# Performance work log

Hardware: AMD Instinct MI355X
Metric: run time of the kernel (lower is better)

Reference implementation:

```python
import jax, jax.numpy as jnp
import numpy as np

K = 3
PAD = 1
GROUPS = 1
BASES = 16


def _conv2d(x, w, b, pad):
    # x: (B, Cin, H, W), w: (Cout, Cin, kh, kw) NCHW/OIHW
    out = jax.lax.conv_general_dilated(
        x, w, window_strides=(1, 1), padding=[(pad, pad), (pad, pad)],
        dimension_numbers=("NCHW", "OIHW", "NCHW"))
    return out + b[None, :, None, None]


def setup_inputs() -> dict:
    key = jax.random.key(0)
    ks = jax.random.split(key, 5)
    B, C, H, Wd = 4, 64, 128, 128
    x = jax.random.normal(ks[0], (B, C, H, Wd), dtype=jnp.float32)
    # basis weight: (1, groups, out_c/g * in_c/g * k^2, bases)
    J = (C // GROUPS) * K * K
    Og = C // GROUPS
    W = jax.random.normal(ks[1], (1, GROUPS, Og * J, BASES), dtype=jnp.float32) * 0.05
    pw = jax.random.normal(ks[2], (BASES, C, 1, 1), dtype=jnp.float32) * 0.05
    pb = jnp.zeros((BASES,), dtype=jnp.float32)
    cw = jax.random.normal(ks[3], (BASES, BASES, 3, 3), dtype=jnp.float32) * 0.05
    cb = jnp.zeros((BASES,), dtype=jnp.float32)
    return {"x": x, "W": W, "pw": pw, "pb": pb, "cw": cw, "cb": cb}


def reference(x, W, pw, pb, cw, cb):
    B, C, H, Wd = x.shape
    P = H * Wd
    g = GROUPS
    Og = C // g          # out channels per group (out_c == in_c here)
    J = (C // g) * K * K  # unfolded patch length per group

    # predictor: 1x1 conv -> relu -> 3x3 conv  => para: (B, bases, P)
    para = _conv2d(x, pw, pb, 0)
    para = jax.nn.relu(para)
    para = _conv2d(para, cw, cb, 1)
    para = para.reshape(B, BASES, P)

    # unfold (im2col): feature dim ordered (c, kh, kw) like F.unfold
    xu = jax.lax.conv_general_dilated_patches(
        x, filter_shape=(K, K), window_strides=(1, 1),
        padding=[(PAD, PAD), (PAD, PAD)])  # (B, C*K*K, H, W)
    xu = xu.reshape(B, g, J, P)

    # per-pixel dynamic weights: weight[b,g,o,j,p] = sum_e Wb[g,o,j,e] * para[b,e,p]
    # out[b,g,o,p] = sum_j weight * xu  -- reassociate: contract j first (small E)
    Wb = W.reshape(g, Og, J, BASES)
    t = jnp.einsum('goje,bgjp->bgoep', Wb, xu)      # (B, g, Og, E, P)
    out = jnp.einsum('bgoep,bep->bgop', t, para)    # (B, g, Og, P)
    return out.reshape(B, C, H, Wd)
```

## Files before the change

kernel.cpp:

```cpp
#include <hip/hip_runtime.h>

typedef __attribute__((ext_vector_type(8))) short short8;
typedef __attribute__((ext_vector_type(8))) __bf16 bf16x8;
typedef __attribute__((ext_vector_type(4))) float f32x4;

#define B_ 4
#define C_ 64
#define H_ 128
#define W_ 128
#define P_ (H_*W_)
#define E_ 16

#define OFF_XT   0u
#define XT_BYTES (4u*130u*130u*64u*2u)
#define OFF_A    8652800u
#define OFF_R1   9832448u

__device__ inline unsigned short f2bf(float f) {
    union { float f; unsigned u; } v; v.f = f;
    unsigned r = v.u + 0x7FFF + ((v.u >> 16) & 1);
    return (unsigned short)(r >> 16);
}

__global__ __launch_bounds__(256) void k_prep(const float* __restrict__ x,
                                              unsigned short* __restrict__ xt,
                                              const float* __restrict__ pw,
                                              const float* __restrict__ pb,
                                              float* __restrict__ r1,
                                              const float* __restrict__ Wsrc,
                                              unsigned short* __restrict__ A) {
    __shared__ float smem[9216];
    int t = threadIdx.x;
    if (blockIdx.x < 256) {
        float* lpw = smem;
        float* lpb = smem + 1024;
        for (int lin = t; lin < 1024; lin += 256) lpw[lin] = pw[lin];
        if (t < 16) lpb[t] = pb[t];
        __syncthreads();

        int rowid = blockIdx.x * 2 + (t >> 7);
        int b = rowid >> 7, y = rowid & 127;
        int tt = t & 127;

        const float* src = x + (size_t)b * C_ * P_ + y * W_ + tt;
        unsigned short* dst = xt + ((size_t)(b * 130 + y + 1) * 130 + tt + 1) * 64;
        float s[16];
#pragma unroll
        for (int e = 0; e < 16; ++e) s[e] = lpb[e];
#pragma unroll
        for (int i = 0; i < 8; ++i) {
            short8 v;
#pragma unroll
            for (int j = 0; j < 8; ++j) {
                float xv = src[(size_t)(i * 8 + j) * P_];
                v[j] = (short)f2bf(xv);
#pragma unroll
                for (int e = 0; e < 16; ++e) s[e] = fmaf(lpw[e * 64 + i * 8 + j], xv, s[e]);
            }
            ((short8*)dst)[i] = v;
        }
        float* rd = r1 + (size_t)b * 16 * P_ + y * 128 + tt;
#pragma unroll
        for (int e = 0; e < 16; ++e) rd[(size_t)e * P_] = fmaxf(s[e], 0.f);

        short8 z = {0,0,0,0,0,0,0,0};
        if (tt < 16) {
            int col = (tt >> 3) * 129, i = tt & 7;
            unsigned short* bp = xt + ((size_t)(b * 130 + y + 1) * 130 + col) * 64;
            ((short8*)bp)[i] = z;
        }
        if (y == 0 || y == 127) {
            int prow = (y == 0) ? 0 : 129;
            unsigned short* rp = xt + (size_t)(b * 130 + prow) * 130 * 64;
            for (int ci = tt; ci < 1040; ci += 128) ((short8*)rp)[ci] = z;
        }
    } else {
        int o = blockIdx.x - 256;
        const float* src = Wsrc + (size_t)o * 9216;
        for (int lin = t; lin < 9216; lin += 256) smem[lin] = src[lin];
        __syncthreads();
        int g = o >> 2, f = o & 3;
        unsigned short* dst = A + ((size_t)g * 72 + f) * 512;
        for (int lin = t; lin < 9216; lin += 256) {
            int ks = lin >> 9, rem = lin & 511;
            int lane = rem >> 3, j = rem & 7;
            int llo = lane & 15, lhi = lane >> 4;
            int col = ks * 32 + lhi * 8 + j;
            int tap = col >> 6, c = col & 63;
            dst[(size_t)ks * 2048 + rem] = f2bf(smem[(c * 9 + tap) * 16 + llo]);
        }
    }
}

__global__ __launch_bounds__(256, 2) void k_main(const unsigned short* __restrict__ xt,
                                                 const unsigned short* __restrict__ A,
                                                 const float* __restrict__ r1,
                                                 const float* __restrict__ cw,
                                                 const float* __restrict__ cb,
                                                 float* __restrict__ out) {
    __shared__ unsigned short lds[3 * 130 * 64];
    __shared__ float lcw2[2304];
    __shared__ float parald[16 * 128];
    int r = blockIdx.x;
    int xcd = r & 7;
    int yl = r >> 3;
    int rowid = xcd * 64 + yl;
    int b = rowid >> 7, y = rowid & 127;

    int tid = threadIdx.x;
    int wave = tid >> 6, lane = tid & 63, lhi = lane >> 4, llo = lane & 15;

    const unsigned short* xrow = xt + (size_t)(b * 130 + y) * 130 * 64;
    for (int ci = tid; ci < 3120; ci += 256) {
        int row = ci / 1040, rem = ci - row * 1040;
        int xx = rem >> 3, cc = rem & 7;
        short8 v = *(const short8*)(xrow + ((size_t)row * 130 + xx) * 64 + cc * 8);
        int lb = row * 16640 + xx * 128 + ((cc * 16) ^ ((xx & 7) << 4));
        *(short8*)((char*)lds + lb) = v;
    }
    for (int lin = tid; lin < 2304; lin += 256) {
        int ep = lin / 144, rem = lin - ep * 144;
        int tap = rem >> 4, e = rem & 15;
        lcw2[lin] = cw[(e * 16 + ep) * 9 + tap];
    }
    __syncthreads();

    {
        int px = tid & 127, eg = tid >> 7;
        const float* r1b = r1 + (size_t)b * 16 * P_;
        float s[8];
#pragma unroll
        for (int ee = 0; ee < 8; ++ee) s[ee] = cb[eg * 8 + ee];
        for (int dy = 0; dy < 3; ++dy) {
            int yy = y + dy - 1;
            if (yy < 0 || yy > 127) continue;
            for (int dx = 0; dx < 3; ++dx) {
                int xx = px + dx - 1;
                if (xx < 0 || xx > 127) continue;
                int tap = dy * 3 + dx;
                const float* rq = r1b + yy * 128 + xx;
                const float* cwt = lcw2 + tap * 16 + eg * 8;
#pragma unroll
                for (int ep = 0; ep < 16; ++ep) {
                    float v = rq[(size_t)ep * P_];
                    const float* cc = cwt + ep * 144;
#pragma unroll
                    for (int ee = 0; ee < 8; ++ee) s[ee] = fmaf(cc[ee], v, s[ee]);
                }
            }
        }
#pragma unroll
        for (int ee = 0; ee < 8; ++ee) parald[(eg * 8 + ee) * 128 + px] = s[ee];
    }
    __syncthreads();

    float* po = out + (size_t)b * 64 * P_ + y * 128;

    int qv[2][3];
#pragma unroll
    for (int kw = 0; kw < 3; ++kw) {
        int rowi = llo + kw;
        int base0 = rowi * 128 + ((lhi * 16) ^ ((rowi & 7) << 4));
        qv[0][kw] = base0;
        qv[1][kw] = base0 ^ 64;
    }
    const char* ldsc = (const char*)lds;

#define PF_AF(dst, KS) do { \
    _Pragma("unroll") \
    for (int f_ = 0; f_ < 4; ++f_) \
        dst[f_] = *(const bf16x8*)(Agl + (KS) * 2048 + f_ * 512); \
    __builtin_amdgcn_sched_barrier(0); \
} while (0)

#define HALF(AFU, AFP, PFKS, PAR, KW) do { \
    PF_AF(AFP, PFKS); \
    const char* bp = bprow + qv[PAR][KW]; \
    bf16x8 bf[8]; \
    _Pragma("unroll") \
    for (int pg_ = 0; pg_ < 8; ++pg_) \
        bf[pg_] = *(const bf16x8*)(bp + pg_ * 2048); \
    __builtin_amdgcn_s_setprio(1); \
    _Pragma("unroll") \
    for (int f_ = 0; f_ < 4; ++f_) \
    _Pragma("unroll") \
    for (int pg_ = 0; pg_ < 8; ++pg_) \
        acc[f_][pg_] = __builtin_amdgcn_mfma_f32_16x16x32_bf16(AFU[f_], bf[pg_], acc[f_][pg_], 0, 0, 0); \
    __builtin_amdgcn_s_setprio(0); \
} while (0)

#pragma unroll 1
    for (int chunk = 0; chunk < 4; ++chunk) {
        int obase = chunk * 16 + wave * 4;
        int g = obase >> 2;
        const unsigned short* Agl = A + (size_t)g * 36864 + lane * 8;

        f32x4 acc[4][8];
#pragma unroll
        for (int f = 0; f < 4; ++f)
#pragma unroll
            for (int pg = 0; pg < 8; ++pg) acc[f][pg] = (f32x4){0.f, 0.f, 0.f, 0.f};

        bf16x8 afA[4], afB[4], afC[4];
        PF_AF(afA, 0);
        PF_AF(afB, 1);

#pragma unroll 1
        for (int kh = 0; kh < 3; ++kh) {
            const int ksc = kh * 6;
            const char* bprow = ldsc + kh * 16640;
            HALF(afA, afC, ksc + 2, 0, 0);
            HALF(afB, afA, ksc + 3, 1, 0);
            HALF(afC, afB, ksc + 4, 0, 1);
            HALF(afA, afC, ksc + 5, 1, 1);
            HALF(afB, afA, ksc + 6, 0, 2);
            HALF(afC, afB, ksc + 7, 1, 2);
        }

        float pvv[8][4];
#pragma unroll
        for (int pg = 0; pg < 8; ++pg)
#pragma unroll
            for (int rr = 0; rr < 4; ++rr)
                pvv[pg][rr] = parald[(lhi * 4 + rr) * 128 + pg * 16 + llo];

#pragma unroll
        for (int f = 0; f < 4; ++f) {
            int o = obase + f;
#pragma unroll
            for (int pg = 0; pg < 8; ++pg) {
                float s = acc[f][pg][0] * pvv[pg][0] + acc[f][pg][1] * pvv[pg][1] +
                          acc[f][pg][2] * pvv[pg][2] + acc[f][pg][3] * pvv[pg][3];
                s += __shfl_xor(s, 16);
                s += __shfl_xor(s, 32);
                if (lhi == 0)
                    __builtin_nontemporal_store(s, &po[(size_t)o * P_ + pg * 16 + llo]);
            }
        }
    }
#undef PF_AF
#undef HALF
}

extern "C" void kernel_launch(void* const* d_in, const int* in_sizes, int n_in,
                              void* d_out, int out_size, void* d_ws, size_t ws_size,
                              hipStream_t stream) {
    const float* x  = (const float*)d_in[0];
    const float* W  = (const float*)d_in[1];
    const float* pw = (const float*)d_in[2];
    const float* pb = (const float*)d_in[3];
    const float* cw = (const float*)d_in[4];
    const float* cb = (const float*)d_in[5];
    float* out = (float*)d_out;
    char* ws = (char*)d_ws;
    unsigned short* xt = (unsigned short*)(ws + OFF_XT);
    unsigned short* Am = (unsigned short*)(ws + OFF_A);
    float* r1   = (float*)(ws + OFF_R1);

    hipLaunchKernelGGL(k_prep, dim3(320), dim3(256), 0, stream, x, xt, pw, pb, r1, W, Am);
    hipLaunchKernelGGL(k_main, dim3(512), dim3(256), 0, stream, xt, Am, r1, cw, cb, out);
}
```

Measured before the change: 85.46 us.

## Fuse input transpose and 1x1 predictor conv into main kernel, drop intermediates

Removes the global bf16 padded NHWC copy of x and the global relu(1x1 conv) intermediate. Each main-kernel block now reads the three fp32 input rows it needs, computes the 1x1 conv plus relu into LDS, then converts the rows to bf16 into the swizzled LDS layout. The prep kernel now only repacks the basis weights. This saves global write and read traffic and work in the prep kernel. In exchange each input row is read and the 1x1 conv recomputed about three times across neighbouring blocks, and LDS use grows to about 67KB per block, which could limit occupancy.

```diff
diff --git a/kernel.cpp b/kernel.cpp
--- a/kernel.cpp
+++ b/kernel.cpp
@@ -11,10 +11,7 @@
 #define P_ (H_*W_)
 #define E_ 16
 
-#define OFF_XT   0u
-#define XT_BYTES (4u*130u*130u*64u*2u)
 #define OFF_A    8652800u
-#define OFF_R1   9832448u
 
 __device__ inline unsigned short f2bf(float f) {
     union { float f; unsigned u; } v; v.f = f;
@@ -22,85 +19,37 @@
     return (unsigned short)(r >> 16);
 }
 
-__global__ __launch_bounds__(256) void k_prep(const float* __restrict__ x,
-                                              unsigned short* __restrict__ xt,
-                                              const float* __restrict__ pw,
-                                              const float* __restrict__ pb,
-                                              float* __restrict__ r1,
-                                              const float* __restrict__ Wsrc,
-                                              unsigned short* __restrict__ A) {
-    __shared__ float smem[9216];
-    int t = threadIdx.x;
-    if (blockIdx.x < 256) {
-        float* lpw = smem;
-        float* lpb = smem + 1024;
-        for (int lin = t; lin < 1024; lin += 256) lpw[lin] = pw[lin];
-        if (t < 16) lpb[t] = pb[t];
-        __syncthreads();
-
-        int rowid = blockIdx.x * 2 + (t >> 7);
-        int b = rowid >> 7, y = rowid & 127;
-        int tt = t & 127;
-
-        const float* src = x + (size_t)b * C_ * P_ + y * W_ + tt;
-        unsigned short* dst = xt + ((size_t)(b * 130 + y + 1) * 130 + tt + 1) * 64;
-        float s[16];
-#pragma unroll
-        for (int e = 0; e < 16; ++e) s[e] = lpb[e];
-#pragma unroll
-        for (int i = 0; i < 8; ++i) {
-            short8 v;
-#pragma unroll
-            for (int j = 0; j < 8; ++j) {
-                float xv = src[(size_t)(i * 8 + j) * P_];
-                v[j] = (short)f2bf(xv);
-#pragma unroll
-                for (int e = 0; e < 16; ++e) s[e] = fmaf(lpw[e * 64 + i * 8 + j], xv, s[e]);
-            }
-            ((short8*)dst)[i] = v;
-        }
-        float* rd = r1 + (size_t)b * 16 * P_ + y * 128 + tt;
-#pragma unroll
-        for (int e = 0; e < 16; ++e) rd[(size_t)e * P_] = fmaxf(s[e], 0.f);
-
-        short8 z = {0,0,0,0,0,0,0,0};
-        if (tt < 16) {
-            int col = (tt >> 3) * 129, i = tt & 7;
-            unsigned short* bp = xt + ((size_t)(b * 130 + y + 1) * 130 + col) * 64;
-            ((short8*)bp)[i] = z;
-        }
-        if (y == 0 || y == 127) {
-            int prow = (y == 0) ? 0 : 129;
-            unsigned short* rp = xt + (size_t)(b * 130 + prow) * 130 * 64;
-            for (int ci = tt; ci < 1040; ci += 128) ((short8*)rp)[ci] = z;
-        }
-    } else {
-        int o = blockIdx.x - 256;
-        const float* src = Wsrc + (size_t)o * 9216;
-        for (int lin = t; lin < 9216; lin += 256) smem[lin] = src[lin];
-        __syncthreads();
-        int g = o >> 2, f = o & 3;
-        unsigned short* dst = A + ((size_t)g * 72 + f) * 512;
-        for (int lin = t; lin < 9216; lin += 256) {
-            int ks = lin >> 9, rem = lin & 511;
-            int lane = rem >> 3, j = rem & 7;
-            int llo = lane & 15, lhi = lane >> 4;
-            int col = ks * 32 + lhi * 8 + j;
-            int tap = col >> 6, c = col & 63;
-            dst[(size_t)ks * 2048 + rem] = f2bf(smem[(c * 9 + tap) * 16 + llo]);
-        }
-    }
-}
-
-__global__ __launch_bounds__(256, 2) void k_main(const unsigned short* __restrict__ xt,
+__global__ __launch_bounds__(256) void k_prepA(const float* __restrict__ Wsrc,
+                                               unsigned short* __restrict__ A) {
+    __shared__ float lw[9216];
+    int o = blockIdx.x, t = threadIdx.x;
+    const float* src = Wsrc + (size_t)o * 9216;
+    for (int lin = t; lin < 9216; lin += 256) lw[lin] = src[lin];
+    __syncthreads();
+    int g = o >> 2, f = o & 3;
+    unsigned short* dst = A + ((size_t)g * 72 + f) * 512;
+    for (int lin = t; lin < 9216; lin += 256) {
+        int ks = lin >> 9, rem = lin & 511;
+        int lane = rem >> 3, j = rem & 7;
+        int llo = lane & 15, lhi = lane >> 4;
+        int col = ks * 32 + lhi * 8 + j;
+        int tap = col >> 6, c = col & 63;
+        dst[(size_t)ks * 2048 + rem] = f2bf(lw[(c * 9 + tap) * 16 + llo]);
+    }
+}
+
+__global__ __launch_bounds__(256, 2) void k_main(const float* __restrict__ x,
                                                  const unsigned short* __restrict__ A,
-                                                 const float* __restrict__ r1,
+                                                 const float* __restrict__ pw,
+                                                 const float* __restrict__ pb,
                                                  const float* __restrict__ cw,
                                                  const float* __restrict__ cb,
                                                  float* __restrict__ out) {
-    __shared__ unsigned short lds[3 * 130 * 64];
-    __shared__ float lcw2[2304];
-    __shared__ float parald[16 * 128];
+    __shared__ __align__(16) char smem[67328];
+    float* r1slab = (float*)smem;
+    float* lcw2   = (float*)(smem + 49920);
+    float* parapw = (float*)(smem + 59136);
+
     int r = blockIdx.x;
     int xcd = r & 7;
     int yl = r >> 3;
@@ -109,15 +58,9 @@
 
     int tid = threadIdx.x;
     int wave = tid >> 6, lane = tid & 63, lhi = lane >> 4, llo = lane & 15;
-
-    const unsigned short* xrow = xt + (size_t)(b * 130 + y) * 130 * 64;
-    for (int ci = tid; ci < 3120; ci += 256) {
-        int row = ci / 1040, rem = ci - row * 1040;
-        int xx = rem >> 3, cc = rem & 7;
-        short8 v = *(const short8*)(xrow + ((size_t)row * 130 + xx) * 64 + cc * 8);
-        int lb = row * 16640 + xx * 128 + ((cc * 16) ^ ((xx & 7) << 4));
-        *(short8*)((char*)lds + lb) = v;
-    }
+    const float* xb = x + (size_t)b * C_ * P_;
+
+    for (int lin = tid; lin < 1024; lin += 256) parapw[lin] = pw[lin];
     for (int lin = tid; lin < 2304; lin += 256) {
         int ep = lin / 144, rem = lin - ep * 144;
         int tap = rem >> 4, e = rem & 15;
@@ -125,32 +68,91 @@
     }
     __syncthreads();
 
+    for (int task = tid; task < 384; task += 256) {
+        int rr = task >> 7, px = task & 127;
+        int yy = y + rr - 1;
+        float* rrow = r1slab + rr * 2048;
+        if (yy >= 0 && yy <= 127) {
+            const float* xs = xb + yy * 128 + px;
+            float s[16];
+#pragma unroll
+            for (int e = 0; e < 16; ++e) s[e] = pb[e];
+            for (int c = 0; c < 64; ++c) {
+                float xv = xs[(size_t)c * P_];
+#pragma unroll
+                for (int e = 0; e < 16; ++e) s[e] = fmaf(parapw[e * 64 + c], xv, s[e]);
+            }
+#pragma unroll
+            for (int e = 0; e < 16; ++e) rrow[e * 128 + px] = fmaxf(s[e], 0.f);
+        } else {
+#pragma unroll
+            for (int e = 0; e < 16; ++e) rrow[e * 128 + px] = 0.f;
+        }
+    }
+    __syncthreads();
+
+    float pout[8];
+    int px2 = tid & 127, eg = tid >> 7;
     {
-        int px = tid & 127, eg = tid >> 7;
-        const float* r1b = r1 + (size_t)b * 16 * P_;
-        float s[8];
-#pragma unroll
-        for (int ee = 0; ee < 8; ++ee) s[ee] = cb[eg * 8 + ee];
+#pragma unroll
+        for (int ee = 0; ee < 8; ++ee) pout[ee] = cb[eg * 8 + ee];
         for (int dy = 0; dy < 3; ++dy) {
-            int yy = y + dy - 1;
-            if (yy < 0 || yy > 127) continue;
             for (int dx = 0; dx < 3; ++dx) {
-                int xx = px + dx - 1;
+                int xx = px2 + dx - 1;
                 if (xx < 0 || xx > 127) continue;
                 int tap = dy * 3 + dx;
-                const float* rq = r1b + yy * 128 + xx;
+                const float* rq = r1slab + dy * 2048 + xx;
                 const float* cwt = lcw2 + tap * 16 + eg * 8;
 #pragma unroll
                 for (int ep = 0; ep < 16; ++ep) {
-                    float v = rq[(size_t)ep * P_];
+                    float v = rq[ep * 128];
                     const float* cc = cwt + ep * 144;
 #pragma unroll
-                    for (int ee = 0; ee < 8; ++ee) s[ee] = fmaf(cc[ee], v, s[ee]);
+                    for (int ee = 0; ee < 8; ++ee) pout[ee] = fmaf(cc[ee], v, pout[ee]);
                 }
             }
         }
-#pragma unroll
-        for (int ee = 0; ee < 8; ++ee) parald[(eg * 8 + ee) * 128 + px] = s[ee];
+    }
+    __syncthreads();
+#pragma unroll
+    for (int ee = 0; ee < 8; ++ee) parapw[(eg * 8 + ee) * 128 + px2] = pout[ee];
+    __syncthreads();
+    const float* parald = parapw;
+
+    {
+        short8 z = {0,0,0,0,0,0,0,0};
+        for (int task = tid; task < 384; task += 256) {
+            int rr = task >> 7, px = task & 127;
+            int yy = y + rr - 1;
+            int xx = px + 1;
+            if (yy >= 0 && yy <= 127) {
+                const float* xs = xb + yy * 128 + px;
+#pragma unroll
+                for (int cc = 0; cc < 8; ++cc) {
+                    short8 v;
+#pragma unroll
+                    for (int j = 0; j < 8; ++j) v[j] = (short)f2bf(xs[(size_t)(cc * 8 + j) * P_]);
+                    int lb = rr * 16640 + xx * 128 + ((cc * 16) ^ ((xx & 7) << 4));
+                    *(short8*)(smem + lb) = v;
+                }
+            } else {
+#pragma unroll
+                for (int cc = 0; cc < 8; ++cc) {
+                    int lb = rr * 16640 + xx * 128 + ((cc * 16) ^ ((xx & 7) << 4));
+                    *(short8*)(smem + lb) = z;
+                }
+            }
+            if (px == 0) {
+#pragma unroll
+                for (int cc = 0; cc < 8; ++cc)
+                    *(short8*)(smem + rr * 16640 + (cc * 16)) = z;
+            }
+            if (px == 127) {
+#pragma unroll
+                for (int cc = 0; cc < 8; ++cc)
+                    *(short8*)(smem + rr * 16640 + 129 * 128 + ((cc * 16) ^ 16)) = z;
+            }
+        }
     }
     __syncthreads();
 
@@ -164,7 +166,7 @@
         qv[0][kw] = base0;
         qv[1][kw] = base0 ^ 64;
     }
-    const char* ldsc = (const char*)lds;
+    const char* ldsc = (const char*)smem;
 
 #define PF_AF(dst, KS) do { \
     _Pragma("unroll") \
@@ -253,10 +255,8 @@
     const float* cb = (const float*)d_in[5];
     float* out = (float*)d_out;
     char* ws = (char*)d_ws;
-    unsigned short* xt = (unsigned short*)(ws + OFF_XT);
     unsigned short* Am = (unsigned short*)(ws + OFF_A);
-    float* r1   = (float*)(ws + OFF_R1);
-
-    hipLaunchKernelGGL(k_prep, dim3(320), dim3(256), 0, stream, x, xt, pw, pb, r1, W, Am);
-    hipLaunchKernelGGL(k_main, dim3(512), dim3(256), 0, stream, xt, Am, r1, cw, cb, out);
-}
+
+    hipLaunchKernelGGL(k_prepA, dim3(64), dim3(256), 0, stream, W, Am);
+    hipLaunchKernelGGL(k_main, dim3(512), dim3(256), 0, stream, x, Am, pw, pb, cw, cb, out);
+}
```

New measurement: 91.51 us. 7.1% more time.

## Switch main GEMM from 16x16x32 to 32x32x16 bf16 MFMA tiles

Applied to the files above, without the earlier changes.

Rewrites the dynamic-conv GEMM inner loop to use 32x32x16 MFMA instructions in place of 16x16x32. The weight prep kernel is relaid to match the new A-operand fragment layout, and the B-operand LDS addressing and epilogue reduction with para are reworked for the 32-lane output layout. Larger MFMA tiles mean fewer A/B operand loads per FLOP and only one cross-lane shuffle per output. In exchange, the K loop is split into many smaller steps with a shallower prefetch pipeline.

```diff
diff --git a/kernel.cpp b/kernel.cpp
--- a/kernel.cpp
+++ b/kernel.cpp
@@ -2,7 +2,7 @@
 
 typedef __attribute__((ext_vector_type(8))) short short8;
 typedef __attribute__((ext_vector_type(8))) __bf16 bf16x8;
-typedef __attribute__((ext_vector_type(4))) float f32x4;
+typedef __attribute__((ext_vector_type(16))) float f32x16;
 
 #define B_ 4
 #define C_ 64
@@ -11,8 +11,6 @@
 #define P_ (H_*W_)
 #define E_ 16
 
-#define OFF_XT   0u
-#define XT_BYTES (4u*130u*130u*64u*2u)
 #define OFF_A    8652800u
 #define OFF_R1   9832448u
 
@@ -79,15 +77,17 @@
         const float* src = Wsrc + (size_t)o * 9216;
         for (int lin = t; lin < 9216; lin += 256) smem[lin] = src[lin];
         __syncthreads();
-        int g = o >> 2, f = o & 3;
-        unsigned short* dst = A + ((size_t)g * 72 + f) * 512;
+        int mt = o >> 1, lo = (o & 1) * 16;
         for (int lin = t; lin < 9216; lin += 256) {
-            int ks = lin >> 9, rem = lin & 511;
-            int lane = rem >> 3, j = rem & 7;
-            int llo = lane & 15, lhi = lane >> 4;
-            int col = ks * 32 + lhi * 8 + j;
+            int kstep = lin >> 8;
+            int rem = lin & 255;
+            int e = rem >> 4, kk = rem & 15;
+            int hi2 = kk >> 3, j = kk & 7;
+            int col = kstep * 16 + kk;
             int tap = col >> 6, c = col & 63;
-            dst[(size_t)ks * 2048 + rem] = f2bf(smem[(c * 9 + tap) * 16 + llo]);
+            int lane = hi2 * 32 + lo + e;
+            A[((size_t)(mt * 36 + kstep)) * 512 + lane * 8 + j] =
+                f2bf(smem[(c * 9 + tap) * 16 + e]);
         }
     }
 }
@@ -108,7 +108,8 @@
     int b = rowid >> 7, y = rowid & 127;
 
     int tid = threadIdx.x;
-    int wave = tid >> 6, lane = tid & 63, lhi = lane >> 4, llo = lane & 15;
+    int wave = tid >> 6, lane = tid & 63;
+    int l31 = lane & 31, hi = lane >> 5;
 
     const unsigned short* xrow = xt + (size_t)(b * 130 + y) * 130 * 64;
     for (int ci = tid; ci < 3120; ci += 256) {
@@ -155,91 +156,93 @@
     __syncthreads();
 
     float* po = out + (size_t)b * 64 * P_ + y * 128;
-
-    int qv[2][3];
-#pragma unroll
-    for (int kw = 0; kw < 3; ++kw) {
-        int rowi = llo + kw;
-        int base0 = rowi * 128 + ((lhi * 16) ^ ((rowi & 7) << 4));
-        qv[0][kw] = base0;
-        qv[1][kw] = base0 ^ 64;
-    }
     const char* ldsc = (const char*)lds;
 
-#define PF_AF(dst, KS) do { \
-    _Pragma("unroll") \
-    for (int f_ = 0; f_ < 4; ++f_) \
-        dst[f_] = *(const bf16x8*)(Agl + (KS) * 2048 + f_ * 512); \
+    float pv[4][8];
+#pragma unroll
+    for (int nt = 0; nt < 4; ++nt)
+#pragma unroll
+        for (int v = 0; v < 8; ++v)
+            pv[nt][v] = parald[((v & 3) + 4 * hi + 8 * (v >> 2)) * 128 + nt * 32 + l31];
+
+#define PF_AF(dst, S) do { \
+    dst[0] = *(const bf16x8*)(Agl + (S) * 512); \
+    dst[1] = *(const bf16x8*)(Agl + 18432 + (S) * 512); \
     __builtin_amdgcn_sched_barrier(0); \
 } while (0)
 
-#define HALF(AFU, AFP, PFKS, PAR, KW) do { \
-    PF_AF(AFP, PFKS); \
-    const char* bp = bprow + qv[PAR][KW]; \
-    bf16x8 bf[8]; \
+#define SUB(AFU, AFP, S, Q) do { \
+    PF_AF(AFP, (S) + 1); \
+    bf16x8 bf[4]; \
     _Pragma("unroll") \
-    for (int pg_ = 0; pg_ < 8; ++pg_) \
-        bf[pg_] = *(const bf16x8*)(bp + pg_ * 2048); \
+    for (int nt_ = 0; nt_ < 4; ++nt_) \
+        bf[nt_] = *(const bf16x8*)(bprow + nt_ * 4096 + (Q)); \
     __builtin_amdgcn_s_setprio(1); \
     _Pragma("unroll") \
-    for (int f_ = 0; f_ < 4; ++f_) \
+    for (int f_ = 0; f_ < 2; ++f_) \
     _Pragma("unroll") \
-    for (int pg_ = 0; pg_ < 8; ++pg_) \
-        acc[f_][pg_] = __builtin_amdgcn_mfma_f32_16x16x32_bf16(AFU[f_], bf[pg_], acc[f_][pg_], 0, 0, 0); \
+    for (int nt_ = 0; nt_ < 4; ++nt_) \
+        acc[f_][nt_] = __builtin_amdgcn_mfma_f32_32x32x16_bf16(AFU[f_], bf[nt_], acc[f_][nt_], 0, 0, 0); \
     __builtin_amdgcn_s_setprio(0); \
 } while (0)
 
 #pragma unroll 1
     for (int chunk = 0; chunk < 4; ++chunk) {
-        int obase = chunk * 16 + wave * 4;
-        int g = obase >> 2;
-        const unsigned short* Agl = A + (size_t)g * 36864 + lane * 8;
-
-        f32x4 acc[4][8];
-#pragma unroll
-        for (int f = 0; f < 4; ++f)
-#pragma unroll
-            for (int pg = 0; pg < 8; ++pg) acc[f][pg] = (f32x4){0.f, 0.f, 0.f, 0.f};
-
-        bf16x8 afA[4], afB[4], afC[4];
+        int mtb = chunk * 8 + wave * 2;
+        const unsigned short* Agl = A + (size_t)mtb * 18432 + lane * 8;
+
+        f32x16 acc[2][4];
+#pragma unroll
+        for (int f = 0; f < 2; ++f)
+#pragma unroll
+            for (int nt = 0; nt < 4; ++nt)
+#pragma unroll
+                for (int vv = 0; vv < 16; ++vv) acc[f][nt][vv] = 0.f;
+
+        bf16x8 afA[2], afB[2];
         PF_AF(afA, 0);
-        PF_AF(afB, 1);
 
 #pragma unroll 1
         for (int kh = 0; kh < 3; ++kh) {
-            const int ksc = kh * 6;
             const char* bprow = ldsc + kh * 16640;
-            HALF(afA, afC, ksc + 2, 0, 0);
-            HALF(afB, afA, ksc + 3, 1, 0);
-            HALF(afC, afB, ksc + 4, 0, 1);
-            HALF(afA, afC, ksc + 5, 1, 1);
-            HALF(afB, afA, ksc + 6, 0, 2);
-            HALF(afC, afB, ksc + 7, 1, 2);
-        }
-
-        float pvv[8][4];
-#pragma unroll
-        for (int pg = 0; pg < 8; ++pg)
-#pragma unroll
-            for (int rr = 0; rr < 4; ++rr)
-                pvv[pg][rr] = parald[(lhi * 4 + rr) * 128 + pg * 16 + llo];
-
-#pragma unroll
-        for (int f = 0; f < 4; ++f) {
-            int o = obase + f;
-#pragma unroll
-            for (int pg = 0; pg < 8; ++pg) {
-                float s = acc[f][pg][0] * pvv[pg][0] + acc[f][pg][1] * pvv[pg][1] +
-                          acc[f][pg][2] * pvv[pg][2] + acc[f][pg][3] * pvv[pg][3];
-                s += __shfl_xor(s, 16);
-                s += __shfl_xor(s, 32);
-                if (lhi == 0)
-                    __builtin_nontemporal_store(s, &po[(size_t)o * P_ + pg * 16 + llo]);
+#pragma unroll 1
+            for (int kw = 0; kw < 3; ++kw) {
+                int xk = l31 + kw;
+                int rb = xk * 128, swz = (xk & 7) << 4, h16 = hi * 16;
+                int q0 = rb + ((h16) ^ swz);
+                int q1 = rb + ((32 + h16) ^ swz);
+                int q2 = rb + ((64 + h16) ^ swz);
+                int q3 = rb + ((96 + h16) ^ swz);
+                int sb = (kh * 3 + kw) * 4;
+                SUB(afA, afB, sb + 0, q0);
+                SUB(afB, afA, sb + 1, q1);
+                SUB(afA, afB, sb + 2, q2);
+                SUB(afB, afA, sb + 3, q3);
+            }
+        }
+
+        int obase = mtb * 2;
+#pragma unroll
+        for (int f = 0; f < 2; ++f) {
+            int oe = obase + 2 * f;
+#pragma unroll
+            for (int nt = 0; nt < 4; ++nt) {
+                float se = 0.f, so = 0.f;
+#pragma unroll
+                for (int v = 0; v < 8; ++v) {
+                    se = fmaf(acc[f][nt][v], pv[nt][v], se);
+                    so = fmaf(acc[f][nt][v + 8], pv[nt][v], so);
+                }
+                se += __shfl_xor(se, 32);
+                so += __shfl_xor(so, 32);
+                int od = hi ? (oe + 1) : oe;
+                float sv = hi ? so : se;
+                __builtin_nontemporal_store(sv, &po[(size_t)od * P_ + nt * 32 + l31]);
             }
         }
     }
 #undef PF_AF
-#undef HALF
+#undef SUB
 }
 
 extern "C" void kernel_launch(void* const* d_in, const int* in_sizes, int n_in,
@@ -253,7 +256,7 @@
     const float* cb = (const float*)d_in[5];
     float* out = (float*)d_out;
     char* ws = (char*)d_ws;
-    unsigned short* xt = (unsigned short*)(ws + OFF_XT);
+    unsigned short* xt = (unsigned short*)ws;
     unsigned short* Am = (unsigned short*)(ws + OFF_A);
     float* r1   = (float*)(ws + OFF_R1);
 
```

New measurement: 90.64 us. 1.06x slower.
